# Performance work log

Hardware: AMD Instinct MI355X
Metric: run time of the kernel (lower is better)

Reference implementation:

```python
import jax, jax.numpy as jnp
import numpy as np

B, N_MM, N_V, N_A = 2, 256, 64, 128
DIM, HEADS, ATTN_RATIO, MLP_RATIO = 1024, 16, 0.25, 4.0
INNER = int(DIM * ATTN_RATIO)          # 256
HID = int(DIM * MLP_RATIO)             # 4096
SCALE = (DIM // HEADS) ** -0.5         # faithful to source: uses dim//num_heads
EPS = 1e-5


def setup_inputs() -> dict:
    key = jax.random.key(0)
    ks = jax.random.split(key, 16)
    s = 0.02
    return {
        "xmm": jax.random.normal(ks[0], (B, N_MM, DIM), jnp.float32),
        "xv": jax.random.normal(ks[1], (B, N_V, DIM), jnp.float32),
        "xa": jax.random.normal(ks[2], (B, N_A, DIM), jnp.float32),
        "ln_mm_w": jnp.ones((DIM,), jnp.float32),
        "ln_mm_b": jnp.zeros((DIM,), jnp.float32),
        "ln_v_w": jnp.ones((DIM,), jnp.float32),
        "ln_v_b": jnp.zeros((DIM,), jnp.float32),
        "ln_a_w": jnp.ones((DIM,), jnp.float32),
        "ln_a_b": jnp.zeros((DIM,), jnp.float32),
        "Wq": jax.random.normal(ks[3], (DIM, INNER), jnp.float32) * s,
        "Wkv": jax.random.normal(ks[4], (2 * DIM, 2 * INNER), jnp.float32) * s,
        "Wproj": jax.random.normal(ks[5], (INNER, DIM), jnp.float32) * s,
        "bproj": jnp.zeros((DIM,), jnp.float32),
        "ln_mlp_w": jnp.ones((DIM,), jnp.float32),
        "ln_mlp_b": jnp.zeros((DIM,), jnp.float32),
        "W1": jax.random.normal(ks[6], (DIM, HID), jnp.float32) * s,
        "b1": jnp.zeros((HID,), jnp.float32),
        "W2": jax.random.normal(ks[7], (HID, DIM), jnp.float32) * s,
        "b2": jnp.zeros((DIM,), jnp.float32),
    }


def _ln(x, w, b):
    m = x.mean(-1, keepdims=True)
    v = ((x - m) ** 2).mean(-1, keepdims=True)
    return (x - m) / jnp.sqrt(v + EPS) * w + b


def reference(xmm, xv, xa, ln_mm_w, ln_mm_b, ln_v_w, ln_v_b, ln_a_w, ln_a_b,
              Wq, Wkv, Wproj, bproj, ln_mlp_w, ln_mlp_b, W1, b1, W2, b2):
    hd = INNER // HEADS
    src_mm = _ln(xmm, ln_mm_w, ln_mm_b)
    src_v = _ln(xv, ln_v_w, ln_v_b)
    src_a = _ln(xa, ln_a_w, ln_a_b)

    # kv(x_va) where x_va = cat([xv broadcast over N_a, xa broadcast over N_v], -1).
    # Equivalent to projecting each stream separately and broadcast-adding:
    kv_v = src_v @ Wkv[:DIM]            # [B, N_v, 2*INNER]
    kv_a = src_a @ Wkv[DIM:]            # [B, N_a, 2*INNER]
    kv = kv_v[:, :, None, :] + kv_a[:, None, :, :]          # [B, N_v, N_a, 2*INNER]
    kv = kv.reshape(B, N_V * N_A, 2, HEADS, hd)
    k = kv[:, :, 0].transpose(0, 2, 1, 3)                   # [B, H, N_va, hd]
    v = kv[:, :, 1].transpose(0, 2, 1, 3)

    q = (src_mm @ Wq).reshape(B, N_MM, HEADS, hd).transpose(0, 2, 1, 3)

    attn = jnp.einsum('bhqd,bhkd->bhqk', q, k) * SCALE
    attn = jax.nn.softmax(attn, axis=-1)
    out = jnp.einsum('bhqk,bhkd->bhqd', attn, v)
    out = out.transpose(0, 2, 1, 3).reshape(B, N_MM, INNER)
    out = out @ Wproj + bproj

    xmm = xmm + out
    h = _ln(xmm, ln_mlp_w, ln_mlp_b)
    h = jax.nn.gelu(h @ W1 + b1, approximate=False) @ W2 + b2
    return xmm + h
```

## Files before the change

### kernel.cpp

```cpp
#include <hip/hip_runtime.h>
#include <hip/hip_bf16.h>
#include <math.h>


typedef unsigned short ushort_t;
typedef __attribute__((ext_vector_type(8))) __bf16 bf16x8;
typedef __attribute__((ext_vector_type(4))) float f32x4;

#define DEVFN static __device__ __forceinline__

DEVFN ushort_t f2bf(float f) {
    unsigned int x = __float_as_uint(f);
    unsigned int r = x + 0x7FFFu + ((x >> 16) & 1u);
    return (ushort_t)(r >> 16);
}
DEVFN void unpack8(uint4 dv, float* dst) {
    unsigned int ws[4] = {dv.x, dv.y, dv.z, dv.w};
#pragma unroll
    for (int i = 0; i < 4; i++) {
        dst[2 * i] = __uint_as_float(ws[i] << 16);
        dst[2 * i + 1] = __uint_as_float(ws[i] & 0xFFFF0000u);
    }
}

DEVFN void ln_body(const float* __restrict__ x, const float* __restrict__ w,
                   const float* __restrict__ b, ushort_t* __restrict__ out,
                   int row) {
    const float4* xr4 = (const float4*)(x + (size_t)row * 1024);
    ushort_t* orow = out + (size_t)row * 1024;
    int tid = threadIdx.x;
    float4 v4 = xr4[tid];
    float s = v4.x + v4.y + v4.z + v4.w;
    float ss = v4.x * v4.x + v4.y * v4.y + v4.z * v4.z + v4.w * v4.w;
#pragma unroll
    for (int off = 32; off > 0; off >>= 1) {
        s += __shfl_down(s, off);
        ss += __shfl_down(ss, off);
    }
    __shared__ float red[8];
    if ((tid & 63) == 0) {
        red[tid >> 6] = s;
        red[4 + (tid >> 6)] = ss;
    }
    __syncthreads();
    s = red[0] + red[1] + red[2] + red[3];
    ss = red[4] + red[5] + red[6] + red[7];
    float mean = s * (1.f / 1024.f);
    float var = ss * (1.f / 1024.f) - mean * mean;
    float rstd = rsqrtf(var + 1e-5f);
    const float4 w4 = ((const float4*)w)[tid];
    const float4 b4 = ((const float4*)b)[tid];
    union { ushort_t u[4]; uint2 v; } pk;
    pk.u[0] = f2bf((v4.x - mean) * rstd * w4.x + b4.x);
    pk.u[1] = f2bf((v4.y - mean) * rstd * w4.y + b4.y);
    pk.u[2] = f2bf((v4.z - mean) * rstd * w4.z + b4.z);
    pk.u[3] = f2bf((v4.w - mean) * rstd * w4.w + b4.w);
    *(uint2*)(&orow[tid * 4]) = pk.v;
}

__global__ __launch_bounds__(256) void ln_kernel(
    const float* __restrict__ x, const float* __restrict__ w,
    const float* __restrict__ b, ushort_t* __restrict__ out) {
    ln_body(x, w, b, out, blockIdx.x);
}

struct LNSeg {
    const float* x; const float* w; const float* b; ushort_t* out; int start;
};
struct TDesc { const float* in; ushort_t* out; int R, C, nx, start; };

DEVFN void transpose_body(TDesc d, int t, ushort_t (*tile)[33]) {
    int bx = (t % d.nx) * 32;
    int by = (t / d.nx) * 32;
    int tx = threadIdx.x & 31;
    int ty = threadIdx.x >> 5;
    for (int i = ty; i < 32; i += 8)
        tile[i][tx] = f2bf(d.in[(size_t)(by + i) * d.C + bx + tx]);
    __syncthreads();
    for (int i = ty; i < 32; i += 8)
        d.out[(size_t)(bx + i) * d.R + by + tx] = tile[tx][i];
}

__global__ __launch_bounds__(256) void prep_kernel(LNSeg l0, LNSeg l1,
                                                   LNSeg l2, TDesc d0,
                                                   TDesc d1) {
    int id = blockIdx.x;
    if (id < 896) {
        LNSeg s = (id >= l2.start) ? l2 : ((id >= l1.start) ? l1 : l0);
        ln_body(s.x, s.w, s.b, s.out, id - s.start);
        return;
    }
    id -= 896;
    __shared__ ushort_t tile[32][33];
    TDesc d = (id >= d1.start) ? d1 : d0;
    transpose_body(d, id - d.start, tile);
}

template <int EPI, typename OutT>
DEVFN void gemm64_core(const ushort_t* __restrict__ A, int lda,
                       const ushort_t* __restrict__ B, int ldb,
                       OutT* __restrict__ C, int ldc,
                       const float* __restrict__ bias,
                       const float* __restrict__ resid, int K, int m0, int n0,
                       ushort_t* As, ushort_t* Bs) {
    constexpr int LS = 72;
    int tid = threadIdx.x;
    int wave = tid >> 6, lane = tid & 63;
    int wm = wave >> 1, wn = wave & 1;
    int quad = lane >> 4, l16 = lane & 15;

    f32x4 acc[2][2];
#pragma unroll
    for (int i = 0; i < 2; i++)
#pragma unroll
        for (int j = 0; j < 2; j++) acc[i][j] = (f32x4){0.f, 0.f, 0.f, 0.f};

    int r = tid >> 3;
    int c = tid & 7;
    const ushort_t* Ap = A + (size_t)(m0 + r) * lda + c * 8;
    const ushort_t* Bp = B + (size_t)(n0 + r) * ldb + c * 8;
    const ushort_t* Ap2 = Ap + (size_t)32 * lda;
    const ushort_t* Bp2 = Bp + (size_t)32 * ldb;
    uint4 ra = *(const uint4*)Ap, ra2 = *(const uint4*)Ap2;
    uint4 rb = *(const uint4*)Bp, rb2 = *(const uint4*)Bp2;

    for (int k0 = 0; k0 < K; k0 += 64) {
        *(uint4*)(&As[r * LS + c * 8]) = ra;
        *(uint4*)(&As[(r + 32) * LS + c * 8]) = ra2;
        *(uint4*)(&Bs[r * LS + c * 8]) = rb;
        *(uint4*)(&Bs[(r + 32) * LS + c * 8]) = rb2;
        __syncthreads();
        if (k0 + 64 < K) {
            ra = *(const uint4*)(Ap + k0 + 64);
            ra2 = *(const uint4*)(Ap2 + k0 + 64);
            rb = *(const uint4*)(Bp + k0 + 64);
            rb2 = *(const uint4*)(Bp2 + k0 + 64);
        }
#pragma unroll
        for (int ks = 0; ks < 2; ks++) {
            bf16x8 af[2], bfr[2];
#pragma unroll
            for (int i = 0; i < 2; i++)
                af[i] = *(const bf16x8*)(
                    &As[(wm * 32 + i * 16 + l16) * LS + ks * 32 + quad * 8]);
#pragma unroll
            for (int j = 0; j < 2; j++)
                bfr[j] = *(const bf16x8*)(
                    &Bs[(wn * 32 + j * 16 + l16) * LS + ks * 32 + quad * 8]);
#pragma unroll
            for (int i = 0; i < 2; i++)
#pragma unroll
                for (int j = 0; j < 2; j++)
                    acc[i][j] = __builtin_amdgcn_mfma_f32_16x16x32_bf16(
                        af[i], bfr[j], acc[i][j], 0, 0, 0);
        }
        __syncthreads();
    }

#pragma unroll
    for (int i = 0; i < 2; i++)
#pragma unroll
        for (int j = 0; j < 2; j++) {
            int col = n0 + wn * 32 + j * 16 + l16;
            int rbase = m0 + wm * 32 + i * 16 + quad * 4;
            float bv = (EPI == 2 || EPI == 3) ? bias[col] : 0.f;
#pragma unroll
            for (int rr = 0; rr < 4; rr++) {
                int row = rbase + rr;
                float vv = acc[i][j][rr] + bv;
                if (EPI == 2) vv = 0.5f * vv * (1.f + erff(vv * 0.70710678118654752f));
                if (EPI == 3) vv += resid[(size_t)row * ldc + col];
                if constexpr (sizeof(OutT) == 2)
                    C[(size_t)row * ldc + col] = (OutT)f2bf(vv);
                else
                    C[(size_t)row * ldc + col] = vv;
            }
        }
}

template <int EPI, typename OutT>
__global__ __launch_bounds__(256) void gemm64(
    const ushort_t* __restrict__ A, int lda, const ushort_t* __restrict__ Bt,
    int ldb, OutT* __restrict__ C, int ldc, const float* __restrict__ bias,
    const float* __restrict__ resid, int Kper, int sliceStride) {
    __shared__ ushort_t As[64 * 72];
    __shared__ ushort_t Bs[64 * 72];
    int z = blockIdx.z;
    gemm64_core<EPI, OutT>(A + (size_t)z * Kper, lda, Bt + (size_t)z * Kper,
                           ldb, C + (size_t)z * sliceStride, ldc, bias, resid,
                           Kper, blockIdx.y * 64, blockIdx.x * 64, As, Bs);
}

struct GSeg {
    const ushort_t* A; const ushort_t* B; ushort_t* C;
    int lda, ldb, ldc, nx, start;
};

__global__ __launch_bounds__(256) void projT_kernel(GSeg s0, GSeg s1, GSeg s2,
                                                    TDesc d0, TDesc d1,
                                                    TDesc d2, int K) {
    __shared__ ushort_t As[64 * 72];
    __shared__ ushort_t Bs[64 * 72];
    int id = blockIdx.x;
    if (id < 80) {
        GSeg s = (id >= s2.start) ? s2 : ((id >= s1.start) ? s1 : s0);
        int t = id - s.start;
        int n0 = (t % s.nx) * 64;
        int m0 = (t / s.nx) * 64;
        gemm64_core<0, ushort_t>(s.A, s.lda, s.B, s.ldb, s.C, s.ldc, nullptr,
                                 nullptr, K, m0, n0, As, Bs);
        return;
    }
    id -= 80;
    TDesc d = (id >= d2.start) ? d2 : ((id >= d1.start) ? d1 : d0);
    transpose_body(d, id - d.start, (ushort_t(*)[33])As);
}

__global__ __launch_bounds__(256) void reduce_mlp2(
    const float* __restrict__ P, const float* __restrict__ y,
    const float* __restrict__ b2, float* __restrict__ out) {
    int i = blockIdx.x * 256 + threadIdx.x;
    const float4* p = (const float4*)P;
    float4 a = p[i], b = p[i + 131072], cc = p[i + 2 * 131072],
           d = p[i + 3 * 131072];
    float4 yy = ((const float4*)y)[i];
    float4 bb = ((const float4*)b2)[i & 255];
    float4 o;
    o.x = a.x + b.x + cc.x + d.x + yy.x + bb.x;
    o.y = a.y + b.y + cc.y + d.y + yy.y + bb.y;
    o.z = a.z + b.z + cc.z + d.z + yy.z + bb.z;
    o.w = a.w + b.w + cc.w + d.w + yy.w + bb.w;
    ((float4*)out)[i] = o;
}

__global__ __launch_bounds__(256) void attn_kernel(
    const ushort_t* __restrict__ q, const ushort_t* __restrict__ kvv,
    const ushort_t* __restrict__ kva, ushort_t* __restrict__ out) {
    int bh = blockIdx.x;
    int b = bh >> 4, h = bh & 15;
    int tid = threadIdx.x;

    __shared__ float Kv[64][16], Vv[64][16], Ka[128][16], Va[128][16];

    {
        int row = tid >> 2, seg = (tid >> 1) & 1, half = tid & 1;
        const ushort_t* src =
            kvv + (size_t)(b * 64 + row) * 512 + seg * 256 + h * 16 + half * 8;
        float* dst = (seg ? Vv[row] : Kv[row]) + half * 8;
        unpack8(*(const uint4*)src, dst);
    }
#pragma unroll
    for (int t2 = 0; t2 < 2; t2++) {
        int t = tid + t2 * 256;
        int row = t >> 2, seg = (t >> 1) & 1, half = t & 1;
        const ushort_t* src =
            kva + (size_t)(b * 128 + row) * 512 + seg * 256 + h * 16 + half * 8;
        float* dst = (seg ? Va[row] : Ka[row]) + half * 8;
        unpack8(*(const uint4*)src, dst);
    }
    __syncthreads();

    int qlocal = tid >> 2;
    int dg = tid & 3;
    int qrow = blockIdx.y * 64 + qlocal;
    const ushort_t* qp = q + (size_t)(b * 256 + qrow) * 256 + h * 16 + dg * 4;
    uint2 qu = *(const uint2*)qp;
    float4 qv;
    qv.x = __uint_as_float(qu.x << 16) * 0.125f;
    qv.y = __uint_as_float(qu.x & 0xFFFF0000u) * 0.125f;
    qv.z = __uint_as_float(qu.y << 16) * 0.125f;
    qv.w = __uint_as_float(qu.y & 0xFFFF0000u) * 0.125f;

    const float4* Kv4 = (const float4*)Kv;
    const float4* Vv4 = (const float4*)Vv;
    const float4* Ka4 = (const float4*)Ka;
    const float4* Va4 = (const float4*)Va;

    float4 ov = {0.f, 0.f, 0.f, 0.f};
    float den = 0.f;
#pragma unroll 8
    for (int i = 0; i < 64; i++) {
        float4 kk = Kv4[i * 4 + dg];
        float part = qv.x * kk.x + qv.y * kk.y + qv.z * kk.z + qv.w * kk.w;
        part += __shfl_xor(part, 1);
        part += __shfl_xor(part, 2);
        float p = __expf(part);
        den += p;
        float4 vv = Vv4[i * 4 + dg];
        ov.x += p * vv.x; ov.y += p * vv.y; ov.z += p * vv.z; ov.w += p * vv.w;
    }
    float4 oa = {0.f, 0.f, 0.f, 0.f};
    float dena = 0.f;
#pragma unroll 8
    for (int i = 0; i < 128; i++) {
        float4 kk = Ka4[i * 4 + dg];
        float part = qv.x * kk.x + qv.y * kk.y + qv.z * kk.z + qv.w * kk.w;
        part += __shfl_xor(part, 1);
        part += __shfl_xor(part, 2);
        float p = __expf(part);
        dena += p;
        float4 vv = Va4[i * 4 + dg];
        oa.x += p * vv.x; oa.y += p * vv.y; oa.z += p * vv.z; oa.w += p * vv.w;
    }

    float rv = 1.f / den, ra = 1.f / dena;
    union { ushort_t u[4]; uint2 v; } pk;
    pk.u[0] = f2bf(ov.x * rv + oa.x * ra);
    pk.u[1] = f2bf(ov.y * rv + oa.y * ra);
    pk.u[2] = f2bf(ov.z * rv + oa.z * ra);
    pk.u[3] = f2bf(ov.w * rv + oa.w * ra);
    *(uint2*)(out + (size_t)(b * 256 + qrow) * 256 + h * 16 + dg * 4) = pk.v;
}

extern "C" void kernel_launch(void* const* d_in, const int* in_sizes, int n_in,
                              void* d_out, int out_size, void* d_ws,
                              size_t ws_size, hipStream_t stream) {
    const float* xmm = (const float*)d_in[0];
    const float* xv = (const float*)d_in[1];
    const float* xa = (const float*)d_in[2];
    const float* ln_mm_w = (const float*)d_in[3];
    const float* ln_mm_b = (const float*)d_in[4];
    const float* ln_v_w = (const float*)d_in[5];
    const float* ln_v_b = (const float*)d_in[6];
    const float* ln_a_w = (const float*)d_in[7];
    const float* ln_a_b = (const float*)d_in[8];
    const float* Wq = (const float*)d_in[9];
    const float* Wkv = (const float*)d_in[10];
    const float* Wproj = (const float*)d_in[11];
    const float* bproj = (const float*)d_in[12];
    const float* ln_mlp_w = (const float*)d_in[13];
    const float* ln_mlp_b = (const float*)d_in[14];
    const float* W1 = (const float*)d_in[15];
    const float* b1 = (const float*)d_in[16];
    const float* W2 = (const float*)d_in[17];
    const float* b2 = (const float*)d_in[18];
    float* outp = (float*)d_out;

    char* w = (char*)d_ws;
    ushort_t* xmmN = (ushort_t*)w;    w += 512 * 1024 * 2;
    ushort_t* xvN = (ushort_t*)w;     w += 128 * 1024 * 2;
    ushort_t* xaN = (ushort_t*)w;     w += 256 * 1024 * 2;
    ushort_t* Wqt = (ushort_t*)w;     w += 256 * 1024 * 2;
    ushort_t* Wkvt = (ushort_t*)w;    w += 512 * 2048 * 2;
    ushort_t* Wprojt = (ushort_t*)w;  w += 1024 * 256 * 2;
    ushort_t* W1t = (ushort_t*)w;     w += 4096 * 1024 * 2;
    ushort_t* W2t = (ushort_t*)w;     w += 1024 * 4096 * 2;
    ushort_t* qout = (ushort_t*)w;    w += 512 * 256 * 2;
    ushort_t* kvvb = (ushort_t*)w;    w += 128 * 512 * 2;
    ushort_t* kvab = (ushort_t*)w;    w += 256 * 512 * 2;
    ushort_t* attnout = (ushort_t*)w; w += 512 * 256 * 2;
    float* y = (float*)w;             w += 512 * 1024 * 4;
    ushort_t* h0 = (ushort_t*)w;      w += 512 * 1024 * 2;
    ushort_t* g = (ushort_t*)w;       w += 512 * 4096 * 2;
    float* P = (float*)w;             w += 4 * 512 * 1024 * 4;

    LNSeg L0{xmm, ln_mm_w, ln_mm_b, xmmN, 0};
    LNSeg L1{xv, ln_v_w, ln_v_b, xvN, 512};
    LNSeg L2{xa, ln_a_w, ln_a_b, xaN, 640};
    TDesc TQ{Wq, Wqt, 1024, 256, 8, 0};
    TDesc TKV{Wkv, Wkvt, 2048, 512, 16, 256};
    prep_kernel<<<896 + 1280, 256, 0, stream>>>(L0, L1, L2, TQ, TKV);

    GSeg G0{xmmN, Wqt, qout, 1024, 1024, 256, 4, 0};
    GSeg G1{xvN, Wkvt, kvvb, 1024, 2048, 512, 8, 32};
    GSeg G2{xaN, Wkvt + 1024, kvab, 1024, 2048, 512, 8, 48};
    TDesc TP{Wproj, Wprojt, 256, 1024, 32, 0};
    TDesc T1{W1, W1t, 1024, 4096, 128, 256};
    TDesc T2{W2, W2t, 4096, 1024, 32, 4352};
    projT_kernel<<<80 + 8448, 256, 0, stream>>>(G0, G1, G2, TP, T1, T2, 1024);

    attn_kernel<<<dim3(32, 4), 256, 0, stream>>>(qout, kvvb, kvab, attnout);

    gemm64<3, float><<<dim3(16, 8, 1), 256, 0, stream>>>(
        attnout, 256, Wprojt, 256, y, 1024, bproj, xmm, 256, 0);

    ln_kernel<<<512, 256, 0, stream>>>(y, ln_mlp_w, ln_mlp_b, h0);

    gemm64<2, ushort_t><<<dim3(64, 8, 1), 256, 0, stream>>>(
        h0, 1024, W1t, 1024, g, 4096, b1, nullptr, 1024, 0);

    gemm64<4, float><<<dim3(16, 8, 4), 256, 0, stream>>>(
        g, 4096, W2t, 4096, P, 1024, nullptr, nullptr, 1024, 512 * 1024);

    reduce_mlp2<<<512, 256, 0, stream>>>(P, y, b2, outp);

    (void)in_sizes; (void)n_in; (void)out_size; (void)ws_size;
}
```

Measured before the change: 187.4 us.

## Use 128x64 tiles with direct global-to-LDS loads for MLP GEMMs

Adds a 128x64-tile GEMM core that stages A and B tiles with global_load_lds 16-byte direct-to-LDS copies. Each wave now computes a 64x32 sub-tile. Both MLP GEMMs (W1 with bias+GELU, and the split-K W2) switch to it, halving block counts and raising operand reuse per block. The GELU epilogue is dropped from the old 64x64 kernel since it is no longer used there. The unpadded 128-byte LDS row stride may cause bank conflicts on fragment reads, and there is still no double buffering.

```diff
diff --git a/kernel.cpp b/kernel.cpp
--- a/kernel.cpp
+++ b/kernel.cpp
@@ -21,6 +21,12 @@
         dst[2 * i] = __uint_as_float(ws[i] << 16);
         dst[2 * i + 1] = __uint_as_float(ws[i] & 0xFFFF0000u);
     }
+}
+
+typedef const __attribute__((address_space(1))) unsigned int* gas_ptr_t;
+typedef __attribute__((address_space(3))) unsigned int* las_ptr_t;
+DEVFN void glds16(const ushort_t* g, ushort_t* l) {
+    __builtin_amdgcn_global_load_lds((gas_ptr_t)g, (las_ptr_t)l, 16, 0, 0);
 }
 
 DEVFN void ln_body(const float* __restrict__ x, const float* __restrict__ w,
@@ -163,12 +169,11 @@
         for (int j = 0; j < 2; j++) {
             int col = n0 + wn * 32 + j * 16 + l16;
             int rbase = m0 + wm * 32 + i * 16 + quad * 4;
-            float bv = (EPI == 2 || EPI == 3) ? bias[col] : 0.f;
+            float bv = (EPI == 3) ? bias[col] : 0.f;
 #pragma unroll
             for (int rr = 0; rr < 4; rr++) {
                 int row = rbase + rr;
                 float vv = acc[i][j][rr] + bv;
-                if (EPI == 2) vv = 0.5f * vv * (1.f + erff(vv * 0.70710678118654752f));
                 if (EPI == 3) vv += resid[(size_t)row * ldc + col];
                 if constexpr (sizeof(OutT) == 2)
                     C[(size_t)row * ldc + col] = (OutT)f2bf(vv);
@@ -189,6 +194,101 @@
     gemm64_core<EPI, OutT>(A + (size_t)z * Kper, lda, Bt + (size_t)z * Kper,
                            ldb, C + (size_t)z * sliceStride, ldc, bias, resid,
                            Kper, blockIdx.y * 64, blockIdx.x * 64, As, Bs);
+}
+
+template <int EPI, typename OutT>
+DEVFN void gemm128_core(const ushort_t* __restrict__ A, int lda,
+                        const ushort_t* __restrict__ B, int ldb,
+                        OutT* __restrict__ C, int ldc,
+                        const float* __restrict__ bias, int K, int m0, int n0,
+                        ushort_t* As, ushort_t* Bs) {
+    int tid = threadIdx.x;
+    int wave = tid >> 6, lane = tid & 63;
+    int wm = wave >> 1, wn = wave & 1;
+    int quad = lane >> 4, l16 = lane & 15;
+
+    f32x4 acc[4][2];
+#pragma unroll
+    for (int i = 0; i < 4; i++)
+#pragma unroll
+        for (int j = 0; j < 2; j++) acc[i][j] = (f32x4){0.f, 0.f, 0.f, 0.f};
+
+    int sr = lane >> 3;
+    int sc = (lane & 7) * 8;
+    const ushort_t* Abase = A + (size_t)(m0 + sr) * lda + sc;
+    const ushort_t* Bbase = B + (size_t)(n0 + sr) * ldb + sc;
+
+    for (int k0 = 0; k0 < K; k0 += 64) {
+#pragma unroll
+        for (int t = 0; t < 4; t++) {
+            int ch = wave * 4 + t;
+            glds16(Abase + (size_t)ch * 8 * lda + k0, As + ch * 512);
+        }
+#pragma unroll
+        for (int t = 0; t < 2; t++) {
+            int ch = wave * 2 + t;
+            glds16(Bbase + (size_t)ch * 8 * ldb + k0, Bs + ch * 512);
+        }
+        __syncthreads();
+#pragma unroll
+        for (int ks = 0; ks < 2; ks++) {
+            bf16x8 af[4], bfr[2];
+#pragma unroll
+            for (int i = 0; i < 4; i++)
+                af[i] = *(const bf16x8*)(
+                    &As[(wm * 64 + i * 16 + l16) * 64 + ks * 32 + quad * 8]);
+#pragma unroll
+            for (int j = 0; j < 2; j++)
+                bfr[j] = *(const bf16x8*)(
+                    &Bs[(wn * 32 + j * 16 + l16) * 64 + ks * 32 + quad * 8]);
+#pragma unroll
+            for (int i = 0; i < 4; i++)
+#pragma unroll
+                for (int j = 0; j < 2; j++)
+                    acc[i][j] = __builtin_amdgcn_mfma_f32_16x16x32_bf16(
+                        af[i], bfr[j], acc[i][j], 0, 0, 0);
+        }
+        __syncthreads();
+    }
+
+#pragma unroll
+    for (int i = 0; i < 4; i++)
+#pragma unroll
+        for (int j = 0; j < 2; j++) {
+            int col = n0 + wn * 32 + j * 16 + l16;
+            int rbase = m0 + wm * 64 + i * 16 + quad * 4;
+            float bv = (EPI == 2) ? bias[col] : 0.f;
+#pragma unroll
+            for (int rr = 0; rr < 4; rr++) {
+                int row = rbase + rr;
+                float vv = acc[i][j][rr] + bv;
+                if (EPI == 2) vv = 0.5f * vv * (1.f + erff(vv * 0.70710678118654752f));
+                if constexpr (sizeof(OutT) == 2)
+                    C[(size_t)row * ldc + col] = (OutT)f2bf(vv);
+                else
+                    C[(size_t)row * ldc + col] = vv;
+            }
+        }
+}
+
+__global__ __launch_bounds__(256) void mlp1_128(
+    const ushort_t* __restrict__ h0, const ushort_t* __restrict__ W1t,
+    const float* __restrict__ b1, ushort_t* __restrict__ g) {
+    __shared__ ushort_t As[128 * 64];
+    __shared__ ushort_t Bs[64 * 64];
+    gemm128_core<2, ushort_t>(h0, 1024, W1t, 1024, g, 4096, b1, 1024,
+                              blockIdx.y * 128, blockIdx.x * 64, As, Bs);
+}
+
+__global__ __launch_bounds__(256) void mlp2_128(
+    const ushort_t* __restrict__ g, const ushort_t* __restrict__ W2t,
+    float* __restrict__ P) {
+    __shared__ ushort_t As[128 * 64];
+    __shared__ ushort_t Bs[64 * 64];
+    int z = blockIdx.z;
+    gemm128_core<4, float>(g + (size_t)z * 1024, 4096, W2t + (size_t)z * 1024,
+                           4096, P + (size_t)z * 512 * 1024, 1024, nullptr,
+                           1024, blockIdx.y * 128, blockIdx.x * 64, As, Bs);
 }
 
 struct GSeg {
@@ -376,11 +476,9 @@
 
     ln_kernel<<<512, 256, 0, stream>>>(y, ln_mlp_w, ln_mlp_b, h0);
 
-    gemm64<2, ushort_t><<<dim3(64, 8, 1), 256, 0, stream>>>(
-        h0, 1024, W1t, 1024, g, 4096, b1, nullptr, 1024, 0);
-
-    gemm64<4, float><<<dim3(16, 8, 4), 256, 0, stream>>>(
-        g, 4096, W2t, 4096, P, 1024, nullptr, nullptr, 1024, 512 * 1024);
+    mlp1_128<<<dim3(64, 4), 256, 0, stream>>>(h0, W1t, b1, g);
+
+    mlp2_128<<<dim3(16, 4, 4), 256, 0, stream>>>(g, W2t, P);
 
     reduce_mlp2<<<512, 256, 0, stream>>>(P, y, b2, outp);
 
```

New measurement: 202.3 us. 1.08x slower.
